# Kernel tuning notes

Measured on AMD Instinct MI355X. Metric: run time of the kernel, lower is better.

The kernel has to match this reference:

```python
import jax, jax.numpy as jnp
import numpy as np

V, D, DFF, L, H, N, K, NB, R = 32000, 512, 2048, 4, 8, 64, 8, 32, 64
B, S = 2, 512
DH = D // H


def _layernorm(x, g, b, eps=1e-5):
    m = x.mean(-1, keepdims=True)
    v = ((x - m) ** 2).mean(-1, keepdims=True)
    return (x - m) * jax.lax.rsqrt(v + eps) * g + b


def _forward(input_ids, token_emb, pos_emb, basis_A, basis_emb, recipe,
             Wq, bq, Wk, bk, Wv, bv, Ws, bs, Wup, bup, Wdown, bdown,
             ln1_g, ln1_b, ln2_g, ln2_b, alpha, lnf_g, lnf_b):
    Bc, Sc = input_ids.shape
    x = token_emb[input_ids] + pos_emb[:Sc][None]          # [B,S,D]
    causal = jnp.tril(jnp.ones((Sc, Sc), dtype=bool))
    neg = jnp.asarray(-jnp.inf, x.dtype)
    scale = jnp.asarray(1.0 / np.sqrt(DH), x.dtype)
    for i in range(L):
        rec = recipe[i]                                    # [N,NB]
        neuron_emb = jax.nn.softmax(rec, -1) @ basis_emb   # [N,D] routing embedding
        # ---- SimpleRouter on norm1(x) ----
        n1 = _layernorm(x, ln1_g[i], ln1_b[i])
        q = (n1 @ Wq[i] + bq[i]).reshape(Bc, Sc, H, DH)
        k = (n1 @ Wk[i] + bk[i]).reshape(Bc, Sc, H, DH)
        v = (n1 @ Wv[i] + bv[i]).reshape(Bc, Sc, H, DH)
        attn = jnp.einsum('bqhd,bkhd->bhqk', q, k) * scale
        attn = jnp.where(causal[None, None], attn, neg)
        attn = jax.nn.softmax(attn, -1)
        ctx = jnp.einsum('bhqk,bkhd->bqhd', attn, v).reshape(Bc, Sc, D)
        query = jnp.concatenate([n1, ctx], -1) @ Ws[i] + bs[i]   # [B,S,D]
        scores = query @ neuron_emb.T                            # [B,S,N]
        topk_scores, topk_idx = jax.lax.top_k(scores, K)
        weights = jax.nn.softmax(topk_scores, -1)                # [B,S,K]
        # ---- BasisResidualFFN on norm2(x) ----
        n2 = _layernorm(x, ln2_g[i], ln2_b[i])
        sel = jax.nn.softmax(rec[topk_idx], -1)                  # [B,S,K,NB]
        token_recipe = (sel * weights[..., None]).sum(2)         # [B,S,NB]
        # delta = x @ W_A @ W_A^T with W_A = token_recipe . basis_A, computed
        # WITHOUT materializing [B,S,D,R] (same math, associativity only)
        proj = jnp.einsum('bsd,ndr->bsnr', n2, basis_A)          # [B,S,NB,R]
        h = jnp.einsum('bsn,bsnr->bsr', token_recipe, proj)      # [B,S,R]
        delta = jnp.einsum('bsn,bsr,ndr->bsd', token_recipe, h, basis_A)
        xf = n2 + alpha[i] * delta
        ff = jax.nn.gelu(xf @ Wup[i] + bup[i], approximate=False) @ Wdown[i] + bdown[i]
        x = x + ff                                               # dropout=0 (eval)
    x = _layernorm(x, lnf_g, lnf_b)
    return x @ token_emb.T                                       # tied head


def setup_inputs() -> dict:
    key = jax.random.key(0)
    ks = iter(jax.random.split(key, 40))
    std = 0.02
    nrm = lambda shape, s=std: jax.random.normal(next(ks), shape, jnp.float32) * s
    input_ids = jax.random.randint(next(ks), (B, S), 0, V)
    basis_A = jax.random.normal(next(ks), (NB, D, R), jnp.float32)
    basis_A = basis_A / jnp.linalg.norm(basis_A.reshape(NB, -1), axis=-1)[:, None, None]
    basis_emb = jax.random.normal(next(ks), (NB, D), jnp.float32)
    basis_emb = basis_emb / jnp.linalg.norm(basis_emb, axis=-1, keepdims=True)
    return dict(
        input_ids=input_ids,
        token_emb=nrm((V, D)), pos_emb=nrm((S, D)),
        basis_A=basis_A, basis_emb=basis_emb,
        recipe=jax.random.normal(next(ks), (L, N, NB), jnp.float32) * 0.5,
        Wq=nrm((L, D, D)), bq=jnp.zeros((L, D)),
        Wk=nrm((L, D, D)), bk=jnp.zeros((L, D)),
        Wv=nrm((L, D, D)), bv=jnp.zeros((L, D)),
        Ws=nrm((L, 2 * D, D)), bs=jnp.zeros((L, D)),
        Wup=nrm((L, D, DFF)), bup=jnp.zeros((L, DFF)),
        Wdown=nrm((L, DFF, D)), bdown=jnp.zeros((L, D)),
        ln1_g=jnp.ones((L, D)), ln1_b=jnp.zeros((L, D)),
        ln2_g=jnp.ones((L, D)), ln2_b=jnp.zeros((L, D)),
        alpha=jnp.full((L,), 0.1, jnp.float32),
        lnf_g=jnp.ones((D,)), lnf_b=jnp.zeros((D,)),
    )


def reference(input_ids, token_emb, pos_emb, basis_A, basis_emb, recipe,
              Wq, bq, Wk, bk, Wv, bv, Ws, bs, Wup, bup, Wdown, bdown,
              ln1_g, ln1_b, ln2_g, ln2_b, alpha, lnf_g, lnf_b):
    return _forward(input_ids, token_emb, pos_emb, basis_A, basis_emb, recipe,
                    Wq, bq, Wk, bk, Wv, bv, Ws, bs, Wup, bup, Wdown, bdown,
                    ln1_g, ln1_b, ln2_g, ln2_b, alpha, lnf_g, lnf_b)
```

## Files before the change

### kernel.cpp

```cpp
#include <hip/hip_runtime.h>
#include <hip/hip_bf16.h>
#include <math.h>

#define V_  32000
#define D_  512
#define DFF_ 2048
#define L_  4
#define H_  8
#define N_  64
#define K_  8
#define NB_ 32
#define R_  64
#define B_  2
#define S_  512
#define T_  1024
#define DH_ 64

typedef short bhalf8 __attribute__((ext_vector_type(8)));
typedef float floatx4 __attribute__((ext_vector_type(4)));

#define GLOAD16(gp, lp) __builtin_amdgcn_global_load_lds( \
    (const __attribute__((address_space(1))) void*)(gp), \
    (__attribute__((address_space(3))) void*)(lp), 16, 0, 0)

__device__ __forceinline__ float gelu_f(float v) {
    return 0.5f * v * (1.0f + erff(v * 0.70710678118654752f));
}

__device__ __forceinline__ unsigned pk2(float a, float b) {
    unsigned ua = (unsigned)__bfloat16_as_ushort(__float2bfloat16(a));
    unsigned ub = (unsigned)__bfloat16_as_ushort(__float2bfloat16(b));
    return ua | (ub << 16);
}

template<int BM, int BN, int WR, int WC, int EPI>
__device__ __forceinline__ void gemm_dev(
    short* __restrict__ lds,
    const __hip_bfloat16* __restrict__ A, int lda, long sA,
    const __hip_bfloat16* __restrict__ Bt, int ldb, long sB,
    const float* __restrict__ bias,
    const float* __restrict__ aux,
    void* __restrict__ Cv, int ldc, long sC,
    int Kdim, int bm, int bn, int z)
{
    constexpr int FM = BM / WR / 16;
    constexpr int FN = BN / WC / 16;
    constexpr int ACH = BM * 8;
    constexpr int BCH = BN * 8;
    constexpr int HALF = (BM + BN) * 64;
    A  += (long)z * sA;
    Bt += (long)z * sB;
    const int tid = threadIdx.x;
    const int w = tid >> 6, lane = tid & 63;
    const int wr = w / WC, wc = w % WC;
    const int moff = wr * (BM / WR), noff = wc * (BN / WC);
    floatx4 acc[FM][FN] = {};

    auto stage = [&](int buf, int k0) {
        char* baseA = (char*)(lds + buf * HALF);
        char* baseB = (char*)(lds + buf * HALF + BM * 64);
        #pragma unroll
        for (int i = 0; i < ACH / 256; i++) {
            int c = tid + i * 256;
            int m = c >> 3, u = (c & 7) ^ (m & 7);
            GLOAD16(A + (long)(bm + m) * lda + k0 + u * 8, baseA + (w * 64 + i * 256) * 16);
        }
        #pragma unroll
        for (int i = 0; i < BCH / 256; i++) {
            int c = tid + i * 256;
            int m = c >> 3, u = (c & 7) ^ (m & 7);
            GLOAD16(Bt + (long)(bn + m) * ldb + k0 + u * 8, baseB + (w * 64 + i * 256) * 16);
        }
    };

    const int nt = Kdim >> 6;
    stage(0, 0);
    __syncthreads();
    int cur = 0;
    for (int t = 0; t < nt; ++t) {
        if (t + 1 < nt) stage(cur ^ 1, (t + 1) * 64);
        const char* baseA = (const char*)(lds + cur * HALF);
        const char* baseB = (const char*)(lds + cur * HALF + BM * 64);
        #pragma unroll
        for (int kk = 0; kk < 2; kk++) {
            bhalf8 af[FM], bf[FN];
            #pragma unroll
            for (int fm = 0; fm < FM; fm++) {
                int row = moff + fm * 16 + (lane & 15);
                int u = (kk * 4 + (lane >> 4)) ^ (row & 7);
                af[fm] = *(const bhalf8*)(baseA + row * 128 + u * 16);
            }
            #pragma unroll
            for (int fn = 0; fn < FN; fn++) {
                int row = noff + fn * 16 + (lane & 15);
                int u = (kk * 4 + (lane >> 4)) ^ (row & 7);
                bf[fn] = *(const bhalf8*)(baseB + row * 128 + u * 16);
            }
            #pragma unroll
            for (int fm = 0; fm < FM; fm++)
                #pragma unroll
                for (int fn = 0; fn < FN; fn++)
                    acc[fm][fn] = __builtin_amdgcn_mfma_f32_16x16x32_bf16(
                        af[fm], bf[fn], acc[fm][fn], 0, 0, 0);
        }
        __syncthreads();
        cur ^= 1;
    }

    float* Cf = (float*)Cv;
    __hip_bfloat16* Cb = (__hip_bfloat16*)Cv;
    __hip_bfloat16* vtb = (EPI == 5) ? (__hip_bfloat16*)(void*)aux : nullptr;
    const long zoff = (long)z * sC;
    const int lr = lane >> 4, lc = lane & 15;
    float alphaV = (EPI == 3) ? bias[0] : 0.f;
    #pragma unroll
    for (int fm = 0; fm < FM; fm++) {
        #pragma unroll
        for (int fn = 0; fn < FN; fn++) {
            int cN = bn + noff + fn * 16 + lc;
            float bv = (EPI == 3 || !bias || (EPI == 6 && z != 0)) ? 0.f : bias[cN];
            #pragma unroll
            for (int i = 0; i < 4; i++) {
                int rM = bm + moff + fm * 16 + lr * 4 + i;
                long idx = zoff + (long)rM * ldc + cN;
                float v = acc[fm][fn][i] + bv;
                if constexpr (EPI == 0) Cf[idx] = v;
                else if constexpr (EPI == 1) Cb[idx] = __float2bfloat16(v);
                else if constexpr (EPI == 2) Cb[idx] = __float2bfloat16(gelu_f(v));
                else if constexpr (EPI == 3)
                    Cb[idx] = __float2bfloat16(aux[idx] + alphaV * acc[fm][fn][i]);
                else if constexpr (EPI == 4) Cf[idx] += v;
                else if constexpr (EPI == 5) {
                    __hip_bfloat16 bvv = __float2bfloat16(v);
                    Cb[idx] = bvv;
                    if (cN >= 1024) {
                        int hh = (cN - 1024) >> 6, dh = (cN - 1024) & 63;
                        int bb = rM >> 9, ss = rM & 511;
                        vtb[(((long)bb * 8 + hh) * 64 + dh) * 512 + ss] = bvv;
                    }
                }
                else if constexpr (EPI == 6) atomicAdd(&Cf[idx], v);
            }
        }
    }
}

template<int BM, int BN, int WR, int WC, int EPI, int SWZ = 0>
__global__ __launch_bounds__(256) void gemm_mfma(
    const __hip_bfloat16* __restrict__ A, int lda, long sA,
    const __hip_bfloat16* __restrict__ Bt, int ldb, long sB,
    const float* __restrict__ bias,
    const float* __restrict__ aux,
    void* __restrict__ Cv, int ldc, long sC,
    int Kdim)
{
    __shared__ short lds[2 * (BM + BN) * 64];
    int bm, bn;
    if constexpr (SWZ == 1) {
        constexpr int MT = T_ / BM;
        constexpr int NP = V_ / BN;
        constexpr int PPX = (NP + 7) / 8;
        int d = blockIdx.x;
        int xcd = d & 7, k = d >> 3;
        int ty = xcd * PPX + (k >> 3);
        if (ty >= NP) return;
        bm = (k & (MT - 1)) * BM;
        bn = ty * BN;
    } else {
        bm = blockIdx.y * BM;
        bn = blockIdx.x * BN;
    }
    gemm_dev<BM, BN, WR, WC, EPI>(lds, A, lda, sA, Bt, ldb, sB, bias, aux,
                                  Cv, ldc, sC, Kdim, bm, bn, blockIdx.z);
}

__global__ __launch_bounds__(256) void mega_gemm(
    const __hip_bfloat16* __restrict__ catB, const __hip_bfloat16* __restrict__ qkvT,
    const float* __restrict__ bqkv, __hip_bfloat16* __restrict__ VtB,
    __hip_bfloat16* __restrict__ qkvB,
    const __hip_bfloat16* __restrict__ WsB, const __hip_bfloat16* __restrict__ neB,
    __hip_bfloat16* __restrict__ WsneK,
    const __hip_bfloat16* __restrict__ n2B, const __hip_bfloat16* __restrict__ projT,
    float* __restrict__ P)
{
    __shared__ short lds[2 * 192 * 64];
    int blk = blockIdx.x;
    if (blk < 384) {
        gemm_dev<64, 64, 2, 2, 5>(lds, catB, 1024, 0, qkvT, D_, 0, bqkv,
                                  (const float*)VtB, qkvB, 1536, 0, D_,
                                  (blk / 24) * 64, (blk % 24) * 64, 0);
    } else if (blk < 400) {
        gemm_dev<64, 64, 2, 2, 1>(lds, WsB, D_, 0, neB, D_, 0, nullptr, nullptr,
                                  WsneK, N_, 0, D_, (blk - 384) * 64, 0, 0);
    } else {
        int local = blk - 400;
        gemm_dev<128, 64, 2, 2, 0>(lds, n2B, D_, 0, projT, D_, (long)R_ * D_,
                                   nullptr, nullptr, P, NB_ * R_, R_, D_,
                                   (local & 7) * 128, 0, local >> 3);
    }
}

__global__ __launch_bounds__(256) void attn_mfma(
    const __hip_bfloat16* __restrict__ qkv,
    const __hip_bfloat16* __restrict__ vt,
    __hip_bfloat16* __restrict__ catB)
{
    __shared__ short pbuf[4][16][72];
    const int tid = threadIdx.x;
    const int w = tid >> 6, lane = tid & 63;
    const int g = lane >> 4, ql = lane & 15;
    const int h = blockIdx.y, b = blockIdx.z;
    const int qbase = blockIdx.x * 64 + w * 16;

    const long qrow = ((long)(b * S_ + qbase + ql)) * 1536 + h * DH_;
    bhalf8 qa0 = *(const bhalf8*)(qkv + qrow + g * 8);
    bhalf8 qa1 = *(const bhalf8*)(qkv + qrow + 32 + g * 8);
    const __hip_bfloat16* kB = qkv + 512;
    const __hip_bfloat16* vbase = vt + ((long)(b * H_ + h)) * DH_ * S_;

    floatx4 o[4] = {};
    float m = -INFINITY, ls = 0.f;
    const float SC = 0.125f * 1.44269504088896f;
    const int nblk = blockIdx.x + 1;

    for (int kvb = 0; kvb < nblk; kvb++) {
        const int kb0 = kvb * 64;
        floatx4 st[4];
        #pragma unroll
        for (int t = 0; t < 4; t++) {
            long krow = ((long)(b * S_ + kb0 + t * 16 + ql)) * 1536 + h * DH_;
            bhalf8 ka0 = *(const bhalf8*)(kB + krow + g * 8);
            bhalf8 ka1 = *(const bhalf8*)(kB + krow + 32 + g * 8);
            floatx4 z = {};
            z = __builtin_amdgcn_mfma_f32_16x16x32_bf16(ka0, qa0, z, 0, 0, 0);
            z = __builtin_amdgcn_mfma_f32_16x16x32_bf16(ka1, qa1, z, 0, 0, 0);
            st[t] = z;
        }
        const int q = qbase + ql;
        float p[4][4];
        float m4 = -INFINITY;
        #pragma unroll
        for (int t = 0; t < 4; t++)
            #pragma unroll
            for (int i = 0; i < 4; i++) {
                int kv = kb0 + t * 16 + g * 4 + i;
                float v = (kv <= q) ? st[t][i] * SC : -INFINITY;
                p[t][i] = v; m4 = fmaxf(m4, v);
            }
        m4 = fmaxf(m4, __shfl_xor(m4, 16));
        m4 = fmaxf(m4, __shfl_xor(m4, 32));
        float mnew = fmaxf(m, m4);
        float corr = exp2f(m - mnew);
        m = mnew;
        float lsum = 0.f;
        #pragma unroll
        for (int t = 0; t < 4; t++)
            #pragma unroll
            for (int i = 0; i < 4; i++) {
                float e = exp2f(p[t][i] - mnew);
                p[t][i] = e; lsum += e;
            }
        lsum += __shfl_xor(lsum, 16);
        lsum += __shfl_xor(lsum, 32);
        ls = ls * corr + lsum;
        unsigned* prow = (unsigned*)&pbuf[w][ql][0];
        #pragma unroll
        for (int t = 0; t < 4; t++) {
            prow[t * 8 + g * 2]     = pk2(p[t][0], p[t][1]);
            prow[t * 8 + g * 2 + 1] = pk2(p[t][2], p[t][3]);
        }
        #pragma unroll
        for (int i = 0; i < 4; i++) {
            float c = __shfl(corr, g * 4 + i);
            #pragma unroll
            for (int dt = 0; dt < 4; dt++) o[dt][i] *= c;
        }
        __syncthreads();
        #pragma unroll
        for (int ks = 0; ks < 2; ks++) {
            bhalf8 pa = *(const bhalf8*)&pbuf[w][ql][ks * 32 + g * 8];
            #pragma unroll
            for (int dt = 0; dt < 4; dt++) {
                bhalf8 vb = *(const bhalf8*)(vbase + (long)(dt * 16 + ql) * S_ + kb0 + ks * 32 + g * 8);
                o[dt] = __builtin_amdgcn_mfma_f32_16x16x32_bf16(pa, vb, o[dt], 0, 0, 0);
            }
        }
        __syncthreads();
    }
    const float inv = 1.f / ls;
    #pragma unroll
    for (int i = 0; i < 4; i++) {
        float iv = __shfl(inv, g * 4 + i);
        int trow = b * S_ + qbase + g * 4 + i;
        #pragma unroll
        for (int dt = 0; dt < 4; dt++)
            catB[(long)trow * 1024 + 512 + h * DH_ + dt * 16 + ql] =
                __float2bfloat16(o[dt][i] * iv);
    }
}

__device__ __forceinline__ void tcvt_dev(const float* in, int ldn, long sIn,
                                         __hip_bfloat16* out, int ldk, long sOut,
                                         int bx, int by, int bz, float (*tsh)[33]) {
    in  += (long)bz * sIn;
    out += (long)bz * sOut;
    int k0 = by * 32, n0 = bx * 32;
    int tx = threadIdx.x & 31, ty = threadIdx.x >> 5;
    #pragma unroll
    for (int r = 0; r < 4; r++) tsh[ty * 4 + r][tx] = in[(long)(k0 + ty * 4 + r) * ldn + n0 + tx];
    __syncthreads();
    #pragma unroll
    for (int r = 0; r < 4; r++)
        out[(long)(n0 + ty * 4 + r) * ldk + k0 + tx] = __float2bfloat16(tsh[tx][ty * 4 + r]);
}

__global__ __launch_bounds__(256) void prologue_kernel(
    const float* __restrict__ temb, __hip_bfloat16* __restrict__ tembB,
    const float* __restrict__ basisA, __hip_bfloat16* __restrict__ projT,
    __hip_bfloat16* __restrict__ deltaT,
    const float* __restrict__ bq, const float* __restrict__ bk,
    const float* __restrict__ bv, float* __restrict__ bqkv,
    const float* __restrict__ Wq, const float* __restrict__ Wk,
    const float* __restrict__ Wv, __hip_bfloat16* __restrict__ qkvT,
    const float* __restrict__ Wup, __hip_bfloat16* __restrict__ WupT,
    const float* __restrict__ Wdn, __hip_bfloat16* __restrict__ WdnT,
    const float* __restrict__ Ws, __hip_bfloat16* __restrict__ WsB,
    const int* __restrict__ ids, const float* __restrict__ pemb,
    float* __restrict__ x)
{
    __shared__ float tsh[32][33];
    const int blk = blockIdx.x, tid = threadIdx.x;
    if (blk < 16000) {
        long i = ((long)blk * 256 + tid) * 4;
        float4 v = *(const float4*)(temb + i);
        tembB[i]     = __float2bfloat16(v.x);
        tembB[i + 1] = __float2bfloat16(v.y);
        tembB[i + 2] = __float2bfloat16(v.z);
        tembB[i + 3] = __float2bfloat16(v.w);
    } else if (blk < 20096) {
        long i = (long)(blk - 16000) * 256 + tid;
        int r = i & 63; int d = (i >> 6) & 511; int n = i >> 15;
        __hip_bfloat16 v = __float2bfloat16(basisA[i]);
        projT[((long)n * R_ + r) * D_ + d] = v;
        deltaT[(long)d * (NB_ * R_) + n * R_ + r] = v;
    } else if (blk < 20120) {
        int i = (blk - 20096) * 256 + tid;
        int l = i / 1536, j = i % 1536;
        float v = (j < 512) ? bq[l * 512 + j] : (j < 1024) ? bk[l * 512 + j - 512]
                                                           : bv[l * 512 + j - 1024];
        bqkv[i] = v;
    } else if (blk < 21144) {
        int lin = blk - 20120;
        tcvt_dev(Wq, D_, (long)D_ * D_, qkvT, D_, (long)1536 * D_,
                 lin & 15, (lin >> 4) & 15, lin >> 8, tsh);
    } else if (blk < 22168) {
        int lin = blk - 21144;
        tcvt_dev(Wk, D_, (long)D_ * D_, qkvT + 512 * 512, D_, (long)1536 * D_,
                 lin & 15, (lin >> 4) & 15, lin >> 8, tsh);
    } else if (blk < 23192) {
        int lin = blk - 22168;
        tcvt_dev(Wv, D_, (long)D_ * D_, qkvT + 1024 * 512, D_, (long)1536 * D_,
                 lin & 15, (lin >> 4) & 15, lin >> 8, tsh);
    } else if (blk < 27288) {
        int lin = blk - 23192;
        tcvt_dev(Wup, DFF_, (long)D_ * DFF_, WupT, D_, (long)D_ * DFF_,
                 lin & 63, (lin >> 6) & 15, lin >> 10, tsh);
    } else if (blk < 31384) {
        int lin = blk - 27288;
        tcvt_dev(Wdn, D_, (long)DFF_ * D_, WdnT, DFF_, (long)DFF_ * D_,
                 lin & 15, (lin >> 4) & 63, lin >> 10, tsh);
    } else if (blk < 33432) {
        long i = ((long)(blk - 31384) * 256 + tid) * 4;
        float4 v = *(const float4*)(Ws + i);
        WsB[i]     = __float2bfloat16(v.x);
        WsB[i + 1] = __float2bfloat16(v.y);
        WsB[i + 2] = __float2bfloat16(v.z);
        WsB[i + 3] = __float2bfloat16(v.w);
    } else {
        int t = blk - 33432;
        int s = t % S_;
        int id = ids[t];
        for (int d = tid; d < D_; d += 256)
            x[(long)t * D_ + d] = temb[(long)id * D_ + d] + pemb[(long)s * D_ + d];
    }
}

__device__ __forceinline__ float wave_sum(float v) {
    #pragma unroll
    for (int off = 1; off < 64; off <<= 1) v += __shfl_xor(v, off);
    return v;
}

__device__ __forceinline__ void ln_wave(const float* __restrict__ row,
                                        const float* __restrict__ g,
                                        const float* __restrict__ b,
                                        float* __restrict__ outf,
                                        __hip_bfloat16* __restrict__ outb,
                                        int ldo, long t) {
    int lane = threadIdx.x & 63;
    float4 a0 = *(const float4*)(row + lane * 8);
    float4 a1 = *(const float4*)(row + lane * 8 + 4);
    float v[8] = {a0.x, a0.y, a0.z, a0.w, a1.x, a1.y, a1.z, a1.w};
    float s = 0.f;
    #pragma unroll
    for (int j = 0; j < 8; j++) s += v[j];
    float mean = wave_sum(s) * (1.0f / D_);
    float vs = 0.f;
    #pragma unroll
    for (int j = 0; j < 8; j++) { v[j] -= mean; vs += v[j] * v[j]; }
    float rstd = rsqrtf(wave_sum(vs) * (1.0f / D_) + 1e-5f);
    float4 g0 = *(const float4*)(g + lane * 8), g1 = *(const float4*)(g + lane * 8 + 4);
    float4 b0 = *(const float4*)(b + lane * 8), b1 = *(const float4*)(b + lane * 8 + 4);
    float gg[8] = {g0.x, g0.y, g0.z, g0.w, g1.x, g1.y, g1.z, g1.w};
    float bb[8] = {b0.x, b0.y, b0.z, b0.w, b1.x, b1.y, b1.z, b1.w};
    float o[8];
    #pragma unroll
    for (int j = 0; j < 8; j++) o[j] = v[j] * rstd * gg[j] + bb[j];
    if (outf) {
        *(float4*)(outf + t * D_ + lane * 8)     = make_float4(o[0], o[1], o[2], o[3]);
        *(float4*)(outf + t * D_ + lane * 8 + 4) = make_float4(o[4], o[5], o[6], o[7]);
    }
    uint4 pkv = make_uint4(pk2(o[0], o[1]), pk2(o[2], o[3]), pk2(o[4], o[5]), pk2(o[6], o[7]));
    *(uint4*)(outb + (long)t * ldo + lane * 8) = pkv;
}

__global__ __launch_bounds__(256) void prep_kernel(
    const float* __restrict__ x,
    const float* __restrict__ ln1g, const float* __restrict__ ln1b,
    const float* __restrict__ ln2g, const float* __restrict__ ln2b,
    const float* __restrict__ rec, const float* __restrict__ bemb,
    const float* __restrict__ bs,
    __hip_bfloat16* __restrict__ catB, float* __restrict__ buf1,
    __hip_bfloat16* __restrict__ n2B,
    __hip_bfloat16* __restrict__ neb, float* __restrict__ sel,
    float* __restrict__ bsne)
{
    int blk = blockIdx.x, tid = threadIdx.x, w = tid >> 6;
    if (blk < 256) {
        long t = blk * 4 + w;
        ln_wave(x + t * D_, ln1g, ln1b, nullptr, catB, 1024, t);
    } else if (blk < 512) {
        long t = (blk - 256) * 4 + w;
        ln_wave(x + t * D_, ln2g, ln2b, buf1, n2B, 512, t);
    } else {
        __shared__ float red[256];
        __shared__ float wsm[NB_];
        int n = blk - 512;
        if (tid == 0) {
            float mx = -1e30f;
            for (int i = 0; i < NB_; i++) mx = fmaxf(mx, rec[n * NB_ + i]);
            float sm = 0.f;
            for (int i = 0; i < NB_; i++) { float e = expf(rec[n * NB_ + i] - mx); wsm[i] = e; sm += e; }
            float inv = 1.f / sm;
            for (int i = 0; i < NB_; i++) wsm[i] *= inv;
        }
        __syncthreads();
        if (tid < NB_) sel[n * NB_ + tid] = wsm[tid];
        float part = 0.f;
        for (int d = tid; d < D_; d += 256) {
            float acc = 0.f;
            #pragma unroll
            for (int nb = 0; nb < NB_; nb++) acc += wsm[nb] * bemb[nb * D_ + d];
            neb[(long)n * D_ + d] = __float2bfloat16(acc);
            part += bs[d] * acc;
        }
        red[tid] = part; __syncthreads();
        for (int off = 128; off; off >>= 1) { if (tid < off) red[tid] += red[tid + off]; __syncthreads(); }
        if (tid == 0) bsne[n] = red[0];
    }
}

__global__ __launch_bounds__(256) void ln_kernel(const float* __restrict__ in,
                                                 const float* __restrict__ g,
                                                 const float* __restrict__ b,
                                                 __hip_bfloat16* __restrict__ outb) {
    long t = blockIdx.x * 4 + (threadIdx.x >> 6);
    ln_wave(in + t * D_, g, b, nullptr, outb, 512, t);
}

__global__ __launch_bounds__(256) void route_hg(
    const __hip_bfloat16* __restrict__ catB, const __hip_bfloat16* __restrict__ WsneK,
    const float* __restrict__ bsne, const float* __restrict__ sel,
    const float* __restrict__ P, __hip_bfloat16* __restrict__ g)
{
    int t = blockIdx.x, tid = threadIdx.x;
    __shared__ float catf[1024];
    __shared__ float part[4][64];
    __shared__ float trl[32];
    __shared__ float hl[64];
    {
        short4 vv = *(const short4*)(catB + (long)t * 1024 + tid * 4);
        catf[tid * 4 + 0] = __bfloat162float(*(__hip_bfloat16*)&vv.x);
        catf[tid * 4 + 1] = __bfloat162float(*(__hip_bfloat16*)&vv.y);
        catf[tid * 4 + 2] = __bfloat162float(*(__hip_bfloat16*)&vv.z);
        catf[tid * 4 + 3] = __bfloat162float(*(__hip_bfloat16*)&vv.w);
    }
    __syncthreads();
    int n = tid & 63, q = tid >> 6;
    {
        const __hip_bfloat16* wp = WsneK + (long)q * 256 * 64 + n;
        const float* cf = catf + q * 256;
        float a0 = 0.f, a1 = 0.f, a2 = 0.f, a3 = 0.f;
        #pragma unroll 16
        for (int j = 0; j < 256; j += 4) {
            a0 = fmaf(cf[j],     __bfloat162float(wp[(j)     * 64]), a0);
            a1 = fmaf(cf[j + 1], __bfloat162float(wp[(j + 1) * 64]), a1);
            a2 = fmaf(cf[j + 2], __bfloat162float(wp[(j + 2) * 64]), a2);
            a3 = fmaf(cf[j + 3], __bfloat162float(wp[(j + 3) * 64]), a3);
        }
        part[q][n] = (a0 + a1) + (a2 + a3);
    }
    __syncthreads();
    if (tid < 64) {
        int lane = tid;
        float myval = part[0][lane] + part[1][lane] + part[2][lane] + part[3][lane] + bsne[lane];
        float topv[K_]; int topi[K_];
        #pragma unroll
        for (int kk = 0; kk < K_; kk++) {
            float v = myval; int idx = lane;
            #pragma unroll
            for (int off = 32; off; off >>= 1) {
                float ov = __shfl_down(v, off);
                int oi = __shfl_down(idx, off);
                if (ov > v || (ov == v && oi < idx)) { v = ov; idx = oi; }
            }
            v = __shfl(v, 0); idx = __shfl(idx, 0);
            topv[kk] = v; topi[kk] = idx;
            if (lane == idx) myval = -INFINITY;
        }
        float mx = topv[0];
        float wgt[K_], sum = 0.f;
        #pragma unroll
        for (int kk = 0; kk < K_; kk++) { wgt[kk] = expf(topv[kk] - mx); sum += wgt[kk]; }
        float inv = 1.f / sum;
        if (lane < NB_) {
            float a = 0.f;
            #pragma unroll
            for (int kk = 0; kk < K_; kk++) a += wgt[kk] * inv * sel[topi[kk] * NB_ + lane];
            trl[lane] = a;
        }
    }
    __syncthreads();
    if (tid < 64) {
        float acc = 0.f;
        const float* p = P + (long)t * 2048 + tid;
        #pragma unroll
        for (int nn = 0; nn < 32; nn++) acc += trl[nn] * p[nn * 64];
        hl[tid] = acc;
    }
    __syncthreads();
    #pragma unroll
    for (int j = 0; j < 8; j++) {
        int idx = tid * 8 + j;
        int nn = idx >> 6, r = idx & 63;
        g[(long)t * 2048 + idx] = __float2bfloat16(trl[nn] * hl[r]);
    }
}

extern "C" void kernel_launch(void* const* d_in, const int* in_sizes, int n_in,
                              void* d_out, int out_size, void* d_ws, size_t ws_size,
                              hipStream_t stream) {
    const int*   ids    = (const int*)d_in[0];
    const float* temb   = (const float*)d_in[1];
    const float* pemb   = (const float*)d_in[2];
    const float* basisA = (const float*)d_in[3];
    const float* bemb   = (const float*)d_in[4];
    const float* recipe = (const float*)d_in[5];
    const float* Wq = (const float*)d_in[6],  *bq = (const float*)d_in[7];
    const float* Wk = (const float*)d_in[8],  *bk = (const float*)d_in[9];
    const float* Wv = (const float*)d_in[10], *bv = (const float*)d_in[11];
    const float* Ws = (const float*)d_in[12], *bs = (const float*)d_in[13];
    const float* Wup = (const float*)d_in[14], *bup = (const float*)d_in[15];
    const float* Wdn = (const float*)d_in[16], *bdn = (const float*)d_in[17];
    const float* ln1g = (const float*)d_in[18], *ln1b = (const float*)d_in[19];
    const float* ln2g = (const float*)d_in[20], *ln2b = (const float*)d_in[21];
    const float* alpha = (const float*)d_in[22];
    const float* lnfg = (const float*)d_in[23], *lnfb = (const float*)d_in[24];
    float* out = (float*)d_out;
    float* W = (float*)d_ws;

    float* x    = W + 0;
    float* buf1 = W + 524288;
    float* bsne = W + 1114112;
    float* sel  = W + 1212416;
    float* P    = W + 1214464;
    float* bqkv = W + 3835904;
    __hip_bfloat16* SB = (__hip_bfloat16*)(W + 3844096);
    __hip_bfloat16* tembB  = SB + 0;
    __hip_bfloat16* qkvT   = SB + 16384000;
    __hip_bfloat16* WsB    = SB + 19529728;
    __hip_bfloat16* WupT   = SB + 21626880;
    __hip_bfloat16* WdnT   = SB + 25821184;
    __hip_bfloat16* projT  = SB + 30015488;
    __hip_bfloat16* deltaT = SB + 31064064;
    __hip_bfloat16* neB    = SB + 32112640;
    __hip_bfloat16* catB   = SB + 32145408;
    __hip_bfloat16* WsneK  = SB + 33193984;
    __hip_bfloat16* n2B    = SB + 33718272;
    __hip_bfloat16* xfB    = SB + 34242560;
    __hip_bfloat16* gB     = SB + 34766848;
    __hip_bfloat16* ffhB   = SB + 36864000;
    __hip_bfloat16* qkvB   = SB + 38961152;
    __hip_bfloat16* VtB    = SB + 40534016;

    dim3 blk(256);
    prologue_kernel<<<34456, blk, 0, stream>>>(
        temb, tembB, basisA, projT, deltaT, bq, bk, bv, bqkv,
        Wq, Wk, Wv, qkvT, Wup, WupT, Wdn, WdnT, Ws, WsB, ids, pemb, x);

    for (int l = 0; l < L_; l++) {
        prep_kernel<<<576, blk, 0, stream>>>(
            x, ln1g + l * D_, ln1b + l * D_, ln2g + l * D_, ln2b + l * D_,
            recipe + (long)l * N_ * NB_, bemb, bs + l * D_,
            catB, buf1, n2B, neB, sel, bsne);
        mega_gemm<<<656, blk, 0, stream>>>(
            catB, qkvT + (long)l * 1536 * 512, bqkv + l * 1536, VtB, qkvB,
            WsB + (long)l * 1024 * 512, neB, WsneK, n2B, projT, P);
        attn_mfma<<<dim3(8, H_, B_), blk, 0, stream>>>(qkvB, VtB, catB);
        route_hg<<<T_, blk, 0, stream>>>(catB, WsneK, bsne, sel, P, gB);
        gemm_mfma<64, 64, 2, 2, 3><<<dim3(8, 16), blk, 0, stream>>>(
            gB, NB_ * R_, 0, deltaT, NB_ * R_, 0, alpha + l, buf1,
            xfB, D_, 0, NB_ * R_);
        gemm_mfma<64, 64, 2, 2, 2><<<dim3(32, 16), blk, 0, stream>>>(
            xfB, D_, 0, WupT + (long)l * D_ * DFF_, D_, 0, bup + l * DFF_, nullptr,
            ffhB, DFF_, 0, D_);
        gemm_mfma<64, 64, 2, 2, 6><<<dim3(8, 16, 2), blk, 0, stream>>>(
            ffhB, DFF_, 1024, WdnT + (long)l * DFF_ * D_, DFF_, 1024, bdn + l * D_, nullptr,
            x, D_, 0, 1024);
    }
    ln_kernel<<<256, blk, 0, stream>>>(x, lnfg, lnfb, n2B);
    gemm_mfma<128, 64, 2, 2, 0, 1><<<dim3(4032), blk, 0, stream>>>(
        n2B, D_, 0, tembB, D_, 0, nullptr, nullptr, out, V_, 0, D_);
}
```

Before: 536.9 us.

## Stage GEMM outputs through LDS for float4 stores, vectorize prologue casts, retile small GEMMs

Adds a new epilogue mode that writes accumulators to shared memory and then emits coalesced float4 global stores. It is used for the projection GEMM and for the large vocab logits GEMM, where output write bandwidth dominates. The prologue fp32-to-bf16 conversions now handle 8 elements per thread with packed 16-byte stores, which cuts the block count. The delta and down-projection GEMMs switch to 32x64 tiles to launch twice as many blocks. The staging path needs an extra LDS round trip and two barriers, and it assumes the 65-float padded stride fits within the LDS buffer.

```diff
diff --git a/kernel.cpp b/kernel.cpp
--- a/kernel.cpp
+++ b/kernel.cpp
@@ -112,6 +112,29 @@
     __hip_bfloat16* vtb = (EPI == 5) ? (__hip_bfloat16*)(void*)aux : nullptr;
     const long zoff = (long)z * sC;
     const int lr = lane >> 4, lc = lane & 15;
+
+    if constexpr (EPI == 7) {
+        float* st = (float*)lds;
+        #pragma unroll
+        for (int fm = 0; fm < FM; fm++)
+            #pragma unroll
+            for (int fn = 0; fn < FN; fn++)
+                #pragma unroll
+                for (int i = 0; i < 4; i++)
+                    st[(moff + fm * 16 + lr * 4 + i) * 65 + noff + fn * 16 + lc] =
+                        acc[fm][fn][i];
+        __syncthreads();
+        #pragma unroll
+        for (int it = 0; it < (BM * BN / 4) / 256; it++) {
+            int slot = it * 256 + tid;
+            int r = slot >> 4, c4 = (slot & 15) * 4;
+            float4 v = *(float4*)&st[r * 65 + c4];
+            *(float4*)&Cf[zoff + (long)(bm + r) * ldc + bn + c4] = v;
+        }
+        __syncthreads();
+        return;
+    }
+
     float alphaV = (EPI == 3) ? bias[0] : 0.f;
     #pragma unroll
     for (int fm = 0; fm < FM; fm++) {
@@ -194,7 +217,7 @@
                                   WsneK, N_, 0, D_, (blk - 384) * 64, 0, 0);
     } else {
         int local = blk - 400;
-        gemm_dev<128, 64, 2, 2, 0>(lds, n2B, D_, 0, projT, D_, (long)R_ * D_,
+        gemm_dev<128, 64, 2, 2, 7>(lds, n2B, D_, 0, projT, D_, (long)R_ * D_,
                                    nullptr, nullptr, P, NB_ * R_, R_, D_,
                                    (local & 7) * 128, 0, local >> 3);
     }
@@ -312,6 +335,14 @@
     #pragma unroll
     for (int r = 0; r < 4; r++)
         out[(long)(n0 + ty * 4 + r) * ldk + k0 + tx] = __float2bfloat16(tsh[tx][ty * 4 + r]);
+}
+
+__device__ __forceinline__ void cvt8(const float* in, __hip_bfloat16* out, long i) {
+    float4 v0 = *(const float4*)(in + i);
+    float4 v1 = *(const float4*)(in + i + 4);
+    uint4 pkv = make_uint4(pk2(v0.x, v0.y), pk2(v0.z, v0.w),
+                           pk2(v1.x, v1.y), pk2(v1.z, v1.w));
+    *(uint4*)(out + i) = pkv;
 }
 
 __global__ __launch_bounds__(256) void prologue_kernel(
@@ -330,54 +361,44 @@
 {
     __shared__ float tsh[32][33];
     const int blk = blockIdx.x, tid = threadIdx.x;
-    if (blk < 16000) {
-        long i = ((long)blk * 256 + tid) * 4;
-        float4 v = *(const float4*)(temb + i);
-        tembB[i]     = __float2bfloat16(v.x);
-        tembB[i + 1] = __float2bfloat16(v.y);
-        tembB[i + 2] = __float2bfloat16(v.z);
-        tembB[i + 3] = __float2bfloat16(v.w);
-    } else if (blk < 20096) {
-        long i = (long)(blk - 16000) * 256 + tid;
+    if (blk < 8000) {
+        cvt8(temb, tembB, ((long)blk * 256 + tid) * 8);
+    } else if (blk < 12096) {
+        long i = (long)(blk - 8000) * 256 + tid;
         int r = i & 63; int d = (i >> 6) & 511; int n = i >> 15;
         __hip_bfloat16 v = __float2bfloat16(basisA[i]);
         projT[((long)n * R_ + r) * D_ + d] = v;
         deltaT[(long)d * (NB_ * R_) + n * R_ + r] = v;
-    } else if (blk < 20120) {
-        int i = (blk - 20096) * 256 + tid;
+    } else if (blk < 12120) {
+        int i = (blk - 12096) * 256 + tid;
         int l = i / 1536, j = i % 1536;
         float v = (j < 512) ? bq[l * 512 + j] : (j < 1024) ? bk[l * 512 + j - 512]
                                                            : bv[l * 512 + j - 1024];
         bqkv[i] = v;
-    } else if (blk < 21144) {
-        int lin = blk - 20120;
+    } else if (blk < 13144) {
+        int lin = blk - 12120;
         tcvt_dev(Wq, D_, (long)D_ * D_, qkvT, D_, (long)1536 * D_,
                  lin & 15, (lin >> 4) & 15, lin >> 8, tsh);
-    } else if (blk < 22168) {
-        int lin = blk - 21144;
+    } else if (blk < 14168) {
+        int lin = blk - 13144;
         tcvt_dev(Wk, D_, (long)D_ * D_, qkvT + 512 * 512, D_, (long)1536 * D_,
                  lin & 15, (lin >> 4) & 15, lin >> 8, tsh);
-    } else if (blk < 23192) {
-        int lin = blk - 22168;
+    } else if (blk < 15192) {
+        int lin = blk - 14168;
         tcvt_dev(Wv, D_, (long)D_ * D_, qkvT + 1024 * 512, D_, (long)1536 * D_,
                  lin & 15, (lin >> 4) & 15, lin >> 8, tsh);
-    } else if (blk < 27288) {
-        int lin = blk - 23192;
+    } else if (blk < 19288) {
+        int lin = blk - 15192;
         tcvt_dev(Wup, DFF_, (long)D_ * DFF_, WupT, D_, (long)D_ * DFF_,
                  lin & 63, (lin >> 6) & 15, lin >> 10, tsh);
-    } else if (blk < 31384) {
-        int lin = blk - 27288;
+    } else if (blk < 23384) {
+        int lin = blk - 19288;
         tcvt_dev(Wdn, D_, (long)DFF_ * D_, WdnT, DFF_, (long)DFF_ * D_,
                  lin & 15, (lin >> 4) & 63, lin >> 10, tsh);
-    } else if (blk < 33432) {
-        long i = ((long)(blk - 31384) * 256 + tid) * 4;
-        float4 v = *(const float4*)(Ws + i);
-        WsB[i]     = __float2bfloat16(v.x);
-        WsB[i + 1] = __float2bfloat16(v.y);
-        WsB[i + 2] = __float2bfloat16(v.z);
-        WsB[i + 3] = __float2bfloat16(v.w);
+    } else if (blk < 24408) {
+        cvt8(Ws, WsB, ((long)(blk - 23384) * 256 + tid) * 8);
     } else {
-        int t = blk - 33432;
+        int t = blk - 24408;
         int s = t % S_;
         int id = ids[t];
         for (int d = tid; d < D_; d += 256)
@@ -604,7 +625,7 @@
     __hip_bfloat16* VtB    = SB + 40534016;
 
     dim3 blk(256);
-    prologue_kernel<<<34456, blk, 0, stream>>>(
+    prologue_kernel<<<25432, blk, 0, stream>>>(
         temb, tembB, basisA, projT, deltaT, bq, bk, bv, bqkv,
         Wq, Wk, Wv, qkvT, Wup, WupT, Wdn, WdnT, Ws, WsB, ids, pemb, x);
 
@@ -618,17 +639,17 @@
             WsB + (long)l * 1024 * 512, neB, WsneK, n2B, projT, P);
         attn_mfma<<<dim3(8, H_, B_), blk, 0, stream>>>(qkvB, VtB, catB);
         route_hg<<<T_, blk, 0, stream>>>(catB, WsneK, bsne, sel, P, gB);
-        gemm_mfma<64, 64, 2, 2, 3><<<dim3(8, 16), blk, 0, stream>>>(
+        gemm_mfma<32, 64, 1, 4, 3><<<dim3(8, 32), blk, 0, stream>>>(
             gB, NB_ * R_, 0, deltaT, NB_ * R_, 0, alpha + l, buf1,
             xfB, D_, 0, NB_ * R_);
         gemm_mfma<64, 64, 2, 2, 2><<<dim3(32, 16), blk, 0, stream>>>(
             xfB, D_, 0, WupT + (long)l * D_ * DFF_, D_, 0, bup + l * DFF_, nullptr,
             ffhB, DFF_, 0, D_);
-        gemm_mfma<64, 64, 2, 2, 6><<<dim3(8, 16, 2), blk, 0, stream>>>(
+        gemm_mfma<32, 64, 1, 4, 6><<<dim3(8, 32, 2), blk, 0, stream>>>(
             ffhB, DFF_, 1024, WdnT + (long)l * DFF_ * D_, DFF_, 1024, bdn + l * D_, nullptr,
             x, D_, 0, 1024);
     }
     ln_kernel<<<256, blk, 0, stream>>>(x, lnfg, lnfb, n2B);
-    gemm_mfma<128, 64, 2, 2, 0, 1><<<dim3(4032), blk, 0, stream>>>(
+    gemm_mfma<128, 64, 2, 2, 7, 1><<<dim3(4032), blk, 0, stream>>>(
         n2B, D_, 0, tembB, D_, 0, nullptr, nullptr, out, V_, 0, D_);
 }
```

After: 534.2 us. Within noise of the previous version (-0.5%).
